# Kernel optimization log

Hardware: AMD Instinct MI355X
Metric: run time of the kernel (lower is better)

## Reference

```python
import jax, jax.numpy as jnp
import numpy as np

LN_EPS = 1e-5   # torch nn.LayerNorm default
OPM_EPS = 1e-3  # module eps


def _layer_norm(x, gamma, beta):
    mu = jnp.mean(x, axis=-1, keepdims=True)
    var = jnp.var(x, axis=-1, keepdims=True)
    return (x - mu) * jax.lax.rsqrt(var + LN_EPS) * gamma + beta


def setup_inputs() -> dict:
    key = jax.random.key(0)
    ks = jax.random.split(key, 4)
    S, N, c_m, c_h, c_z = 128, 384, 256, 32, 128
    return {
        "m": jax.random.normal(ks[0], (S, N, c_m), dtype=jnp.float32),
        "mask": jnp.ones((S, N), dtype=jnp.float32),
        "ln_gamma": jnp.ones((c_m,), dtype=jnp.float32),
        "ln_beta": jnp.zeros((c_m,), dtype=jnp.float32),
        "w1": jax.random.normal(ks[1], (c_m, c_h), dtype=jnp.float32) / np.sqrt(c_m),
        "b1": jnp.zeros((c_h,), dtype=jnp.float32),
        "w2": jax.random.normal(ks[2], (c_m, c_h), dtype=jnp.float32) / np.sqrt(c_m),
        "b2": jnp.zeros((c_h,), dtype=jnp.float32),
        "w_out": jax.random.normal(ks[3], (c_h * c_h, c_z), dtype=jnp.float32) / np.sqrt(c_h * c_h),
        "b_out": jnp.zeros((c_z,), dtype=jnp.float32),
    }


def reference(m, mask, ln_gamma, ln_beta, w1, b1, w2, b2, w_out, b_out):
    # m: [S, N, C_m], mask: [S, N]
    ln = _layer_norm(m, ln_gamma, ln_beta)                      # [S, N, C_m]
    a = (ln @ w1 + b1) * mask[..., None]                        # [S, N, C_h]
    b = (ln @ w2 + b2) * mask[..., None]                        # [S, N, C_h]
    a = jnp.swapaxes(a, -2, -3)                                 # [N, S, C_h]
    b = jnp.swapaxes(b, -2, -3)                                 # [N, S, C_h]
    norm = jnp.einsum('si,sj->ij', mask, mask)[..., None] + OPM_EPS  # [N, N, 1]
    outer = jnp.einsum('isc,jsd->ijcd', a, b)                   # [N, N, C_h, C_h]
    outer = outer.reshape(outer.shape[:-2] + (-1,))             # [N, N, C_h^2]
    out = outer @ w_out + b_out                                 # [N, N, C_z]
    return out / norm
```

## Files before the change

kernel.cpp:

```cpp
#include <hip/hip_runtime.h>
#include <hip/hip_bf16.h>

#define S_ 128
#define N_ 384
#define CM 256
#define CH 32
#define CZ 128

typedef __attribute__((ext_vector_type(8))) __bf16 bf16x8;
typedef __attribute__((ext_vector_type(4))) float f32x4;

union pack4 { __hip_bfloat16 h[4]; uint2 u; };

__global__ __launch_bounds__(384) void k_prep(const float* __restrict__ w1,
                                              const float* __restrict__ w2,
                                              const float* __restrict__ wout,
                                              const float* __restrict__ mask,
                                              __hip_bfloat16* __restrict__ wt12,
                                              __hip_bfloat16* __restrict__ woutT,
                                              float* __restrict__ RN)
{
    const int b = blockIdx.x, t = threadIdx.x;
    if (b < 64) {
        if (t < 256) {
            const float* w = (b < CH) ? w1 : w2;
            wt12[b * CM + t] = __float2bfloat16(w[(size_t)t * CH + (b & 31)]);
        }
    } else if (b < 192) {
        const int z = b - 64;
        for (int cd = t; cd < CH*CH; cd += 384)
            woutT[(size_t)z * (CH*CH) + cd] = __float2bfloat16(wout[(size_t)cd * CZ + z]);
    } else {
        const int i = b - 192, j = t;
        float acc = 0.f;
        #pragma unroll 8
        for (int s = 0; s < S_; ++s)
            acc += mask[s*N_ + i] * mask[s*N_ + j];
        RN[i*N_ + j] = 1.0f / (acc + 1e-3f);
    }
}

#define LNR 264
__global__ __launch_bounds__(256) void k_lnp(
    const float* __restrict__ m, const float* __restrict__ mask,
    const float* __restrict__ gamma, const float* __restrict__ beta,
    const float* __restrict__ b1, const float* __restrict__ b2,
    const __hip_bfloat16* __restrict__ wt12,
    __hip_bfloat16* __restrict__ At, __hip_bfloat16* __restrict__ Bt)
{
    __shared__ __hip_bfloat16 lnS[128 * LNR];
    __shared__ float msk[128];
    const int n0 = blockIdx.x * 16, s0 = blockIdx.y * 8;
    const int t = threadIdx.x, wave = t >> 6, lane = t & 63;
    const int l15 = lane & 15, quad = lane >> 4;

    if (t < 128) msk[t] = mask[(s0 + (t & 7))*N_ + n0 + (t >> 3)];

    float4 g  = ((const float4*)gamma)[lane];
    float4 be = ((const float4*)beta)[lane];
    for (int i = 0; i < 32; ++i) {
        const int row = wave*32 + i;
        const int n = row >> 3, s = row & 7;
        float4 x = ((const float4*)(m + ((size_t)((s0+s)*N_ + n0 + n)) * CM))[lane];
        float sum = x.x + x.y + x.z + x.w;
        float ssq = x.x*x.x + x.y*x.y + x.z*x.z + x.w*x.w;
        #pragma unroll
        for (int off = 32; off >= 1; off >>= 1) {
            sum += __shfl_xor(sum, off, 64);
            ssq += __shfl_xor(ssq, off, 64);
        }
        const float mean = sum * (1.0f/CM);
        const float var  = ssq * (1.0f/CM) - mean*mean;
        const float rstd = rsqrtf(var + 1e-5f);
        pack4 pk;
        pk.h[0] = __float2bfloat16((x.x - mean)*rstd*g.x + be.x);
        pk.h[1] = __float2bfloat16((x.y - mean)*rstd*g.y + be.y);
        pk.h[2] = __float2bfloat16((x.z - mean)*rstd*g.z + be.z);
        pk.h[3] = __float2bfloat16((x.w - mean)*rstd*g.w + be.w);
        *(uint2*)&lnS[row*LNR + lane*4] = pk.u;
    }
    __syncthreads();

    f32x4 acc[2][4];
    const f32x4 z4 = {0.f,0.f,0.f,0.f};
    #pragma unroll
    for (int mt = 0; mt < 2; ++mt)
        #pragma unroll
        for (int nt = 0; nt < 4; ++nt) acc[mt][nt] = z4;

    #pragma unroll
    for (int kk = 0; kk < 8; ++kk) {
        bf16x8 a0 = *(const bf16x8*)&lnS[(wave*32      + l15)*LNR + kk*32 + quad*8];
        bf16x8 a1 = *(const bf16x8*)&lnS[(wave*32 + 16 + l15)*LNR + kk*32 + quad*8];
        #pragma unroll
        for (int nt = 0; nt < 4; ++nt) {
            bf16x8 wv = *(const bf16x8*)&wt12[(size_t)(nt*16 + l15)*CM + kk*32 + quad*8];
            acc[0][nt] = __builtin_amdgcn_mfma_f32_16x16x32_bf16(a0, wv, acc[0][nt], 0,0,0);
            acc[1][nt] = __builtin_amdgcn_mfma_f32_16x16x32_bf16(a1, wv, acc[1][nt], 0,0,0);
        }
    }

    #pragma unroll
    for (int nt = 0; nt < 4; ++nt) {
        const int ncol = nt*16 + l15;
        const int sel = ncol >> 5, c = ncol & 31;
        const float bias = sel ? b2[c] : b1[c];
        __hip_bfloat16* dst = sel ? Bt : At;
        #pragma unroll
        for (int mt = 0; mt < 2; ++mt) {
            const int rowb = wave*32 + mt*16 + quad*4;
            const int n_loc = rowb >> 3, s_loc = rowb & 7;
            pack4 pk;
            #pragma unroll
            for (int r = 0; r < 4; ++r)
                pk.h[r] = __float2bfloat16((acc[mt][nt][r] + bias) * msk[rowb + r]);
            *(uint2*)&dst[((size_t)(n0 + n_loc)*CH + c)*S_ + s0 + s_loc] = pk.u;
        }
    }
}

#define OR 1160
__global__ __launch_bounds__(512) void k_opm(
    const __hip_bfloat16* __restrict__ At, const __hip_bfloat16* __restrict__ Bt,
    const float* __restrict__ RN, const __hip_bfloat16* __restrict__ woutT,
    const float* __restrict__ bout, float* __restrict__ out)
{
    __shared__ __hip_bfloat16 O[64 * OR];
    const int t = threadIdx.x;
    const int wave = t >> 6, lane = t & 63;
    const int l15 = lane & 15, quad = lane >> 4;
    const int i0 = blockIdx.x * 8, j0 = blockIdx.y * 8;
    const int mhalf = wave & 1, nquad = wave >> 1;

    f32x4 acc[4][8];
    const f32x4 z4 = {0.f,0.f,0.f,0.f};
    #pragma unroll
    for (int nt = 0; nt < 4; ++nt)
        #pragma unroll
        for (int mt = 0; mt < 8; ++mt) acc[nt][mt] = z4;

    const __hip_bfloat16* Ag[8];
    #pragma unroll
    for (int mt = 0; mt < 8; ++mt) {
        const int Mrow = mhalf*128 + mt*16 + l15;
        Ag[mt] = At + ((size_t)(i0 + (Mrow >> 5)) * CH + (Mrow & 31)) * S_ + quad*8;
    }
    const __hip_bfloat16* Bg[4];
    #pragma unroll
    for (int nt = 0; nt < 4; ++nt) {
        const int Ncol = nquad*64 + nt*16 + l15;
        Bg[nt] = Bt + ((size_t)(j0 + (Ncol >> 5)) * CH + (Ncol & 31)) * S_ + quad*8;
    }

    #pragma unroll
    for (int kk = 0; kk < 4; ++kk) {
        bf16x8 af[8], bfr[4];
        #pragma unroll
        for (int mt = 0; mt < 8; ++mt) af[mt] = *(const bf16x8*)(Ag[mt] + kk*32);
        #pragma unroll
        for (int nt = 0; nt < 4; ++nt) bfr[nt] = *(const bf16x8*)(Bg[nt] + kk*32);
        #pragma unroll
        for (int nt = 0; nt < 4; ++nt)
            #pragma unroll
            for (int mt = 0; mt < 8; ++mt)
                acc[nt][mt] = __builtin_amdgcn_mfma_f32_16x16x32_bf16(
                    bfr[nt], af[mt], acc[nt][mt], 0, 0, 0);
    }

    #pragma unroll
    for (int mt = 0; mt < 8; ++mt) {
        const int Mcol = mhalf*128 + mt*16 + l15;
        const int i_l = Mcol >> 5, c = Mcol & 31;
        #pragma unroll
        for (int nt = 0; nt < 4; ++nt) {
            const int Nrow = nquad*64 + nt*16 + quad*4;
            const int j_l = Nrow >> 5, d0 = Nrow & 31;
            const int p = i_l*8 + j_l;
            pack4 pk;
            #pragma unroll
            for (int r = 0; r < 4; ++r) pk.h[r] = __float2bfloat16(acc[nt][mt][r]);
            *(uint2*)&O[p*OR + c*36 + d0] = pk.u;
        }
    }
    __syncthreads();

    const int zb = wave * 16;
    f32x4 oacc[4];
    #pragma unroll
    for (int mt = 0; mt < 4; ++mt) oacc[mt] = z4;

    #pragma unroll
    for (int h = 0; h < 2; ++h) {
        bf16x8 wf[16];
        #pragma unroll
        for (int k2 = 0; k2 < 16; ++k2)
            wf[k2] = *(const bf16x8*)&woutT[(size_t)(zb + l15) * (CH*CH)
                                            + (h*16 + k2)*32 + quad*8];
        #pragma unroll
        for (int k2 = 0; k2 < 16; ++k2) {
            const int kk = h*16 + k2;
            #pragma unroll
            for (int mt = 0; mt < 4; ++mt) {
                bf16x8 a = *(const bf16x8*)&O[(mt*16 + l15)*OR + kk*36 + quad*8];
                oacc[mt] = __builtin_amdgcn_mfma_f32_16x16x32_bf16(
                    a, wf[k2], oacc[mt], 0, 0, 0);
            }
        }
    }

    const int zc = zb + l15;
    const float bz = bout[zc];
    #pragma unroll
    for (int mt = 0; mt < 4; ++mt) {
        #pragma unroll
        for (int r = 0; r < 4; ++r) {
            const int p = mt*16 + quad*4 + r;
            const int i = i0 + (p >> 3), j = j0 + (p & 7);
            const float rn = RN[i*N_ + j];
            out[((size_t)(i*N_ + j))*CZ + zc] = (oacc[mt][r] + bz) * rn;
        }
    }
}

extern "C" void kernel_launch(void* const* d_in, const int* in_sizes, int n_in,
                              void* d_out, int out_size, void* d_ws, size_t ws_size,
                              hipStream_t stream)
{
    const float* m    = (const float*)d_in[0];
    const float* mask = (const float*)d_in[1];
    const float* gam  = (const float*)d_in[2];
    const float* bet  = (const float*)d_in[3];
    const float* w1   = (const float*)d_in[4];
    const float* b1   = (const float*)d_in[5];
    const float* w2   = (const float*)d_in[6];
    const float* b2   = (const float*)d_in[7];
    const float* wout = (const float*)d_in[8];
    const float* bout = (const float*)d_in[9];
    float* out = (float*)d_out;

    __hip_bfloat16* At    = (__hip_bfloat16*)d_ws;
    __hip_bfloat16* Bt    = At + (size_t)N_ * CH * S_;
    __hip_bfloat16* woutT = Bt + (size_t)N_ * CH * S_;
    __hip_bfloat16* wt12  = woutT + (size_t)CZ * CH * CH;
    float*          RN    = (float*)(wt12 + (size_t)64 * CM);

    k_prep<<<576, 384, 0, stream>>>(w1, w2, wout, mask, wt12, woutT, RN);
    dim3 gl(24, 16);
    k_lnp<<<gl, 256, 0, stream>>>(m, mask, gam, bet, b1, b2, wt12, At, Bt);
    dim3 grid(N_ / 8, N_ / 8);
    k_opm<<<grid, 512, 0, stream>>>(At, Bt, RN, woutT, bout, out);
}
```

Baseline: 323.6 us.

## Double k_opm block to 1024 threads, splitting each wave's outer-product and projection tiles

The outer-product kernel now runs 16 waves per block instead of 8. Each wave computes a 64x64 tile of the outer product instead of 128x64, and half the pixel rows for its output-channel slice in the projection stage. The aim is more latency hiding and fewer accumulator registers per thread with the same shared-memory tile. In exchange, each wout fragment is loaded by twice as many waves and the register budget per thread is tighter under the 1024-thread launch bound.

Result: slower. 412.7 us (+27.5%).

```diff
diff --git a/kernel.cpp b/kernel.cpp
--- a/kernel.cpp
+++ b/kernel.cpp
@@ -120,7 +120,7 @@
 }
 
 #define OR 1160
-__global__ __launch_bounds__(512) void k_opm(
+__global__ __launch_bounds__(1024) void k_opm(
     const __hip_bfloat16* __restrict__ At, const __hip_bfloat16* __restrict__ Bt,
     const float* __restrict__ RN, const __hip_bfloat16* __restrict__ woutT,
     const float* __restrict__ bout, float* __restrict__ out)
@@ -130,50 +130,50 @@
     const int wave = t >> 6, lane = t & 63;
     const int l15 = lane & 15, quad = lane >> 4;
     const int i0 = blockIdx.x * 8, j0 = blockIdx.y * 8;
-    const int mhalf = wave & 1, nquad = wave >> 1;
-
-    f32x4 acc[4][8];
+    const int mq = wave & 3, nq = wave >> 2;
+
+    f32x4 acc[4][4];
     const f32x4 z4 = {0.f,0.f,0.f,0.f};
     #pragma unroll
     for (int nt = 0; nt < 4; ++nt)
         #pragma unroll
-        for (int mt = 0; mt < 8; ++mt) acc[nt][mt] = z4;
-
-    const __hip_bfloat16* Ag[8];
-    #pragma unroll
-    for (int mt = 0; mt < 8; ++mt) {
-        const int Mrow = mhalf*128 + mt*16 + l15;
+        for (int mt = 0; mt < 4; ++mt) acc[nt][mt] = z4;
+
+    const __hip_bfloat16* Ag[4];
+    #pragma unroll
+    for (int mt = 0; mt < 4; ++mt) {
+        const int Mrow = mq*64 + mt*16 + l15;
         Ag[mt] = At + ((size_t)(i0 + (Mrow >> 5)) * CH + (Mrow & 31)) * S_ + quad*8;
     }
     const __hip_bfloat16* Bg[4];
     #pragma unroll
     for (int nt = 0; nt < 4; ++nt) {
-        const int Ncol = nquad*64 + nt*16 + l15;
+        const int Ncol = nq*64 + nt*16 + l15;
         Bg[nt] = Bt + ((size_t)(j0 + (Ncol >> 5)) * CH + (Ncol & 31)) * S_ + quad*8;
     }
 
     #pragma unroll
     for (int kk = 0; kk < 4; ++kk) {
-        bf16x8 af[8], bfr[4];
-        #pragma unroll
-        for (int mt = 0; mt < 8; ++mt) af[mt] = *(const bf16x8*)(Ag[mt] + kk*32);
+        bf16x8 af[4], bfr[4];
+        #pragma unroll
+        for (int mt = 0; mt < 4; ++mt) af[mt] = *(const bf16x8*)(Ag[mt] + kk*32);
         #pragma unroll
         for (int nt = 0; nt < 4; ++nt) bfr[nt] = *(const bf16x8*)(Bg[nt] + kk*32);
         #pragma unroll
         for (int nt = 0; nt < 4; ++nt)
             #pragma unroll
-            for (int mt = 0; mt < 8; ++mt)
+            for (int mt = 0; mt < 4; ++mt)
                 acc[nt][mt] = __builtin_amdgcn_mfma_f32_16x16x32_bf16(
                     bfr[nt], af[mt], acc[nt][mt], 0, 0, 0);
     }
 
     #pragma unroll
-    for (int mt = 0; mt < 8; ++mt) {
-        const int Mcol = mhalf*128 + mt*16 + l15;
+    for (int mt = 0; mt < 4; ++mt) {
+        const int Mcol = mq*64 + mt*16 + l15;
         const int i_l = Mcol >> 5, c = Mcol & 31;
         #pragma unroll
         for (int nt = 0; nt < 4; ++nt) {
-            const int Nrow = nquad*64 + nt*16 + quad*4;
+            const int Nrow = nq*64 + nt*16 + quad*4;
             const int j_l = Nrow >> 5, d0 = Nrow & 31;
             const int p = i_l*8 + j_l;
             pack4 pk;
@@ -184,10 +184,10 @@
     }
     __syncthreads();
 
-    const int zb = wave * 16;
-    f32x4 oacc[4];
-    #pragma unroll
-    for (int mt = 0; mt < 4; ++mt) oacc[mt] = z4;
+    const int zs = wave >> 1, ph = wave & 1;
+    const int zb = zs * 16;
+    f32x4 oacc[2];
+    oacc[0] = z4; oacc[1] = z4;
 
     #pragma unroll
     for (int h = 0; h < 2; ++h) {
@@ -200,10 +200,11 @@
         for (int k2 = 0; k2 < 16; ++k2) {
             const int kk = h*16 + k2;
             #pragma unroll
-            for (int mt = 0; mt < 4; ++mt) {
-                bf16x8 a = *(const bf16x8*)&O[(mt*16 + l15)*OR + kk*36 + quad*8];
-                oacc[mt] = __builtin_amdgcn_mfma_f32_16x16x32_bf16(
-                    a, wf[k2], oacc[mt], 0, 0, 0);
+            for (int mt2 = 0; mt2 < 2; ++mt2) {
+                bf16x8 a = *(const bf16x8*)&O[(ph*32 + mt2*16 + l15)*OR
+                                              + kk*36 + quad*8];
+                oacc[mt2] = __builtin_amdgcn_mfma_f32_16x16x32_bf16(
+                    a, wf[k2], oacc[mt2], 0, 0, 0);
             }
         }
     }
@@ -211,13 +212,13 @@
     const int zc = zb + l15;
     const float bz = bout[zc];
     #pragma unroll
-    for (int mt = 0; mt < 4; ++mt) {
+    for (int mt2 = 0; mt2 < 2; ++mt2) {
         #pragma unroll
         for (int r = 0; r < 4; ++r) {
-            const int p = mt*16 + quad*4 + r;
+            const int p = ph*32 + mt2*16 + quad*4 + r;
             const int i = i0 + (p >> 3), j = j0 + (p & 7);
             const float rn = RN[i*N_ + j];
-            out[((size_t)(i*N_ + j))*CZ + zc] = (oacc[mt][r] + bz) * rn;
+            out[((size_t)(i*N_ + j))*CZ + zc] = (oacc[mt2][r] + bz) * rn;
         }
     }
 }
@@ -248,5 +249,5 @@
     dim3 gl(24, 16);
     k_lnp<<<gl, 256, 0, stream>>>(m, mask, gam, bet, b1, b2, wt12, At, Bt);
     dim3 grid(N_ / 8, N_ / 8);
-    k_opm<<<grid, 512, 0, stream>>>(At, Bt, RN, woutT, bout, out);
-}
+    k_opm<<<grid, 1024, 0, stream>>>(At, Bt, RN, woutT, bout, out);
+}
```
